# Kernel tuning notes

Hardware: AMD Instinct MI355X
Metric: run time of the kernel (lower is better)

Reference implementation:

```python
import jax, jax.numpy as jnp
import numpy as np

B, S, D, H, DFF = 8, 1024, 1024, 16, 4096
DK = D // H
NEG = -1000000000.0


def layernorm(x, g, b, eps=1e-5):
    mu = jnp.mean(x, axis=-1, keepdims=True)
    var = jnp.mean((x - mu) ** 2, axis=-1, keepdims=True)
    return (x - mu) / jnp.sqrt(var + eps) * g + b


def setup_inputs() -> dict:
    key = jax.random.key(0)
    ks = jax.random.split(key, 16)
    s = 0.02
    inp = {
        "x": jax.random.normal(ks[0], (B, S, D), jnp.float32),
        "binary_mask": jax.random.randint(ks[1], (B, S), 0, 2, jnp.int32),
        # per-head projections stacked: [H, D, DK]
        "Wq": jax.random.normal(ks[2], (H, D, DK), jnp.float32) * s,
        "bq": jnp.zeros((H, DK), jnp.float32),
        "Wk": jax.random.normal(ks[3], (H, D, DK), jnp.float32) * s,
        "bk": jnp.zeros((H, DK), jnp.float32),
        "Wv": jax.random.normal(ks[4], (H, D, DK), jnp.float32) * s,
        "bv": jnp.zeros((H, DK), jnp.float32),
        "Wo": jax.random.normal(ks[5], (D, D), jnp.float32) * s,
        "bo": jnp.zeros((D,), jnp.float32),
        "ga": jnp.ones((D,), jnp.float32),
        "ba": jnp.zeros((D,), jnp.float32),
        "W1": jax.random.normal(ks[6], (D, DFF), jnp.float32) * s,
        "b1": jnp.zeros((DFF,), jnp.float32),
        "W2": jax.random.normal(ks[7], (DFF, D), jnp.float32) * s,
        "b2": jnp.zeros((D,), jnp.float32),
        "gf": jnp.ones((D,), jnp.float32),
        "bf": jnp.zeros((D,), jnp.float32),
    }
    return inp


def encoder_fwd(x, binary_mask, Wq, bq, Wk, bk, Wv, bv, Wo, bo, ga, ba, W1, b1, W2, b2, gf, bf):
    # --- multi-head self-attention (heads vectorized over h axis) ---
    q = jnp.einsum("bsd,hdk->bhsk", x, Wq) + bq[None, :, None, :]
    k = jnp.einsum("bsd,hdk->bhsk", x, Wk) + bk[None, :, None, :]
    v = jnp.einsum("bsd,hdk->bhsk", x, Wv) + bv[None, :, None, :]
    score = jnp.einsum("bhik,bhjk->bhij", q, k) / jnp.sqrt(jnp.float32(DK))
    # mask: binary_mask is over KEY positions, broadcast over query dim
    score = score + jnp.where(binary_mask[:, None, None, :] == 0, NEG, 0.0)
    # NOTE: original code softmaxes over dim=1 of [B,Sq,Sk] -> the QUERY axis
    probs = jax.nn.softmax(score, axis=2)
    ctx = jnp.einsum("bhij,bhjk->bhik", probs, v)  # [B,H,S,DK]
    ctx = jnp.transpose(ctx, (0, 2, 1, 3)).reshape(x.shape[0], x.shape[1], D)
    attn_out = ctx @ Wo + bo
    y = layernorm(x + attn_out, ga, ba)
    # --- FFN ---
    h = jax.nn.relu(y @ W1 + b1)
    ffn_out = h @ W2 + b2
    return layernorm(y + ffn_out, gf, bf)


def reference(x, binary_mask, Wq, bq, Wk, bk, Wv, bv, Wo, bo, ga, ba, W1, b1, W2, b2, gf, bf):
    return encoder_fwd(x, binary_mask, Wq, bq, Wk, bk, Wv, bv, Wo, bo, ga, ba, W1, b1, W2, b2, gf, bf)
```

## Files before the change

### kernel.cpp

```cpp
#include <hip/hip_runtime.h>
#include <hip/hip_bf16.h>

typedef __bf16 bf16;
typedef __bf16 bf16x8 __attribute__((ext_vector_type(8)));
typedef __bf16 bf16x4 __attribute__((ext_vector_type(4)));
typedef float  f32x4  __attribute__((ext_vector_type(4)));

#define NB 8
#define NS 1024
#define ND 1024
#define NH 16
#define NDK 64
#define NDFF 4096

static __device__ __forceinline__ f32x4 mfma16(bf16x8 a, bf16x8 b, f32x4 c) {
    return __builtin_amdgcn_mfma_f32_16x16x32_bf16(a, b, c, 0, 0, 0);
}

#define GLDS(g, l) __builtin_amdgcn_global_load_lds( \
    (const __attribute__((address_space(1))) void*)(g), \
    (__attribute__((address_space(3))) void*)(l), 16, 0, 0)

__global__ __launch_bounds__(256) void cvt_x(const float* __restrict__ in,
                                             bf16* __restrict__ out, int n4)
{
    int idx = blockIdx.x * 256 + threadIdx.x;
    if (idx >= n4) return;
    float4 v = ((const float4*)in)[idx];
    bf16x4 o = { (bf16)v.x, (bf16)v.y, (bf16)v.z, (bf16)v.w };
    ((bf16x4*)out)[idx] = o;
}

__global__ __launch_bounds__(256) void prep_transpose(
    const float* __restrict__ Wq, const float* __restrict__ Wk, const float* __restrict__ Wv,
    const float* __restrict__ Wo, const float* __restrict__ W1, const float* __restrict__ W2,
    bf16* __restrict__ wqkvT, bf16* __restrict__ WoT,
    bf16* __restrict__ W1T, bf16* __restrict__ W2T)
{
    __shared__ float T[64][65];
    int bid = blockIdx.x;
    const float* src; bf16* dst; int srcLd, dstLd, tR, tC; bool scale = false;
    if (bid < 768) {
        int mat = bid >> 4, ty = bid & 15;
        int h = mat & 15, type = mat >> 4;
        const float* W = (type == 0) ? Wq : (type == 1 ? Wk : Wv);
        src = W + (size_t)h * ND * NDK;
        srcLd = NDK; tR = ty * 64; tC = 0;
        dst = wqkvT + ((size_t)type * 1024 + h * 64) * ND;
        dstLd = ND;
        scale = (type == 0);
    } else if (bid < 1024) {
        int b2 = bid - 768; int ty = b2 >> 4, tx = b2 & 15;
        src = Wo; srcLd = ND; tR = ty * 64; tC = tx * 64; dst = WoT; dstLd = ND;
    } else if (bid < 2048) {
        int b2 = bid - 1024; int ty = b2 >> 6, tx = b2 & 63;
        src = W1; srcLd = NDFF; tR = ty * 64; tC = tx * 64; dst = W1T; dstLd = ND;
    } else {
        int b2 = bid - 2048; int ty = b2 >> 4, tx = b2 & 15;
        src = W2; srcLd = ND; tR = ty * 64; tC = tx * 64; dst = W2T; dstLd = NDFF;
    }
    int t = threadIdx.x;
    int c0 = t & 63, r0 = t >> 6;
    #pragma unroll
    for (int rr = 0; rr < 16; rr++) {
        int row = rr * 4 + r0;
        T[row][c0] = src[(size_t)(tR + row) * srcLd + tC + c0];
    }
    __syncthreads();
    #pragma unroll
    for (int cc = 0; cc < 16; cc++) {
        int col = cc * 4 + r0;
        float v = T[c0][col];
        if (scale) v *= 0.125f;
        dst[(size_t)(tC + col) * dstLd + tR + c0] = (bf16)v;
    }
}

__global__ void prep_bias(const float* __restrict__ bq, const float* __restrict__ bk,
                          const float* __restrict__ bv, float* __restrict__ bqkv)
{
    int n = blockIdx.x * 256 + threadIdx.x;
    if (n >= 3072) return;
    int type = n >> 10, hk = n & 1023;
    const float* bb = (type == 0) ? bq : (type == 1 ? bk : bv);
    float v = bb[hk];
    if (type == 0) v *= 0.125f;
    bqkv[n] = v;
}

__device__ __forceinline__ void gemm_bt_core(
    const bf16* __restrict__ A, const bf16* __restrict__ BT, int K,
    int rowBase, int colBase, f32x4 (&acc)[4][4], bf16* As, bf16* Bs)
{
    const int tid = threadIdx.x;
    const int lane = tid & 63, wid = tid >> 6;
    const int wr = (wid >> 1) * 64, wc = (wid & 1) * 64;
    const int lrow = lane & 15, lq = lane >> 4;
    const int srow = wid * 32 + (lane >> 3);
    const int gblk = (lane & 7) ^ ((lane >> 3) & 7);
    const bf16* Arow = A + (size_t)(rowBase + srow) * K + gblk * 8;
    const bf16* Brow = BT + (size_t)(colBase + srow) * K + gblk * 8;
    const int co0 = ((lq) ^ (lrow & 7)) * 8;
    const int co1 = ((4 + lq) ^ (lrow & 7)) * 8;
    f32x4 zz = {0.f, 0.f, 0.f, 0.f};
    #pragma unroll
    for (int i = 0; i < 4; i++)
        #pragma unroll
        for (int j = 0; j < 4; j++) acc[i][j] = zz;
    for (int k0 = 0; k0 < K; k0 += 64) {
        __syncthreads();
        #pragma unroll
        for (int it = 0; it < 4; it++)
            GLDS(Arow + (size_t)it * 8 * K + k0, As + (wid * 32 + it * 8) * 64);
        #pragma unroll
        for (int it = 0; it < 4; it++)
            GLDS(Brow + (size_t)it * 8 * K + k0, Bs + (wid * 32 + it * 8) * 64);
        __syncthreads();
        #pragma unroll
        for (int kh = 0; kh < 2; kh++) {
            const int co = kh ? co1 : co0;
            bf16x8 af[4], bfr[4];
            #pragma unroll
            for (int tt = 0; tt < 4; tt++) {
                af[tt]  = *(const bf16x8*)&As[(wr + tt * 16 + lrow) * 64 + co];
                bfr[tt] = *(const bf16x8*)&Bs[(wc + tt * 16 + lrow) * 64 + co];
            }
            #pragma unroll
            for (int i = 0; i < 4; i++)
                #pragma unroll
                for (int j = 0; j < 4; j++)
                    acc[i][j] = mfma16(af[i], bfr[j], acc[i][j]);
        }
    }
}

__global__ __launch_bounds__(256) void g1_qkv(
    const bf16* __restrict__ x, const bf16* __restrict__ wqkvT, const float* __restrict__ bqkv,
    bf16* __restrict__ Q, bf16* __restrict__ Kb, bf16* __restrict__ Vb)
{
    __shared__ bf16 As[128 * 64], Bs[128 * 64];
    f32x4 acc[4][4];
    int rowBase = blockIdx.x * 128, colBase = blockIdx.y * 128;
    gemm_bt_core(x, wqkvT, ND, rowBase, colBase, acc, As, Bs);
    const int tid = threadIdx.x, lane = tid & 63, wid = tid >> 6;
    const int wr = (wid >> 1) * 64, wc = (wid & 1) * 64, lrow = lane & 15, lq = lane >> 4;
    #pragma unroll
    for (int j = 0; j < 4; j++) {
        int gcol = colBase + wc + j * 16 + lrow;
        float bias = bqkv[gcol];
        int type = gcol >> 10, h = (gcol >> 6) & 15, kk = gcol & 63;
        bf16* dst = (type == 0) ? Q : (type == 1 ? Kb : Vb);
        #pragma unroll
        for (int i = 0; i < 4; i++) {
            #pragma unroll
            for (int r = 0; r < 4; r++) {
                int grow = rowBase + wr + i * 16 + lq * 4 + r;
                int b = grow >> 10, s = grow & 1023;
                int bh = b * NH + h;
                dst[((size_t)bh * NS + s) * NDK + kk] = (bf16)(acc[i][j][r] + bias);
            }
        }
    }
}

__global__ __launch_bounds__(256) void vt_trans(
    const bf16* __restrict__ Vb, bf16* __restrict__ Vt)
{
    __shared__ bf16 T[64 * 72];
    int bh = blockIdx.y, s0 = blockIdx.x * 64;
    const bf16* src = Vb + ((size_t)bh * NS + s0) * NDK;
    int tid = threadIdx.x;
    #pragma unroll
    for (int it = 0; it < 2; it++) {
        int g = tid + it * 256;
        int row = g >> 3, c = (g & 7) * 8;
        *(bf16x8*)&T[row * 72 + c] = *(const bf16x8*)&src[row * NDK + c];
    }
    __syncthreads();
    #pragma unroll
    for (int it = 0; it < 2; it++) {
        int g = tid + it * 256;
        int kk = g >> 3, sc = (g & 7) * 8;
        bf16x8 v;
        #pragma unroll
        for (int t = 0; t < 8; t++) v[t] = T[(sc + t) * 72 + kk];
        *(bf16x8*)&Vt[((size_t)bh * NDK + kk) * NS + s0 + sc] = v;
    }
}

__global__ __launch_bounds__(256) void g2_stats(
    const bf16* __restrict__ Q, const bf16* __restrict__ Kb,
    const int* __restrict__ mask, float2* __restrict__ alpha)
{
    __shared__ bf16 Qs[64 * 64];
    int bh = blockIdx.y, b = bh >> 4;
    int jBase = blockIdx.x * 128;
    const bf16* Kp = Kb + (size_t)bh * NS * NDK;
    const bf16* Qp = Q + (size_t)bh * NS * NDK;
    const int tid = threadIdx.x, lane = tid & 63, wid = tid >> 6;
    const int lrow = lane & 15, lq = lane >> 4;
    bf16x8 kf[2][2];
    #pragma unroll
    for (int jt = 0; jt < 2; jt++)
        #pragma unroll
        for (int kh = 0; kh < 2; kh++)
            kf[jt][kh] = *(const bf16x8*)&Kp[(size_t)(jBase + wid * 32 + jt * 16 + lrow) * NDK + kh * 32 + lq * 8];
    const int srow = lane >> 3;
    const int gblk = (lane & 7) ^ srow;
    float Lacc[2][4];
    #pragma unroll
    for (int jt = 0; jt < 2; jt++)
        #pragma unroll
        for (int r = 0; r < 4; r++) Lacc[jt][r] = 0.f;
    f32x4 zz = {0.f, 0.f, 0.f, 0.f};
    for (int i0 = 0; i0 < NS; i0 += 64) {
        __syncthreads();
        #pragma unroll
        for (int it = 0; it < 2; it++)
            GLDS(Qp + (size_t)(i0 + wid * 16 + it * 8 + srow) * NDK + gblk * 8,
                 Qs + (wid * 16 + it * 8) * 64);
        __syncthreads();
        #pragma unroll
        for (int it = 0; it < 4; it++) {
            bf16x8 qb[2];
            #pragma unroll
            for (int kh = 0; kh < 2; kh++)
                qb[kh] = *(const bf16x8*)&Qs[(it * 16 + lrow) * 64 + ((kh * 4 + lq) ^ (lrow & 7)) * 8];
            #pragma unroll
            for (int jt = 0; jt < 2; jt++) {
                f32x4 s = mfma16(kf[jt][0], qb[0], zz);
                s = mfma16(kf[jt][1], qb[1], s);
                #pragma unroll
                for (int r = 0; r < 4; r++) Lacc[jt][r] += __expf(s[r]);
            }
        }
    }
    #pragma unroll
    for (int jt = 0; jt < 2; jt++) {
        #pragma unroll
        for (int r = 0; r < 4; r++) {
            float v = Lacc[jt][r];
            v += __shfl_xor(v, 1); v += __shfl_xor(v, 2);
            v += __shfl_xor(v, 4); v += __shfl_xor(v, 8);
            if (lrow == 0) {
                int j = jBase + wid * 32 + jt * 16 + lq * 4 + r;
                int m = mask[b * NS + j];
                float2 ac;
                ac.x = m ? 1.f / v : 0.f;
                ac.y = m ? 0.f : (1.f / 1024.f);
                alpha[(size_t)bh * NS + j] = ac;
            }
        }
    }
}

__global__ __launch_bounds__(256) void g3_ctx(
    const bf16* __restrict__ Q, const bf16* __restrict__ Kb, const bf16* __restrict__ Vt,
    const float2* __restrict__ alpha, bf16* __restrict__ ctx)
{
    __shared__ bf16 Ks[64 * 64];
    __shared__ bf16 Vs[64 * 64];
    __shared__ bf16 Ps[128 * 64];
    int bh = blockIdx.y, iBase = blockIdx.x * 128;
    int b = bh >> 4, h = bh & 15;
    const bf16* Qp = Q + (size_t)bh * NS * NDK;
    const bf16* Kp = Kb + (size_t)bh * NS * NDK;
    const bf16* Vp = Vt + (size_t)bh * NDK * NS;
    const float2* al = alpha + (size_t)bh * NS;
    const int tid = threadIdx.x, lane = tid & 63, wid = tid >> 6;
    const int lrow = lane & 15, lq = lane >> 4;
    const int wi = wid >> 1, wsub = wid & 1;
    bf16x8 qf[4][2];
    #pragma unroll
    for (int it = 0; it < 4; it++)
        #pragma unroll
        for (int kh = 0; kh < 2; kh++)
            qf[it][kh] = *(const bf16x8*)&Qp[(size_t)(iBase + wi * 64 + it * 16 + lrow) * NDK + kh * 32 + lq * 8];
    const int srow = lane >> 3;
    const int gblk = (lane & 7) ^ srow;
    f32x4 cacc[4][2];
    f32x4 zz = {0.f, 0.f, 0.f, 0.f};
    #pragma unroll
    for (int it = 0; it < 4; it++)
        #pragma unroll
        for (int kt = 0; kt < 2; kt++) cacc[it][kt] = zz;
    for (int j0 = 0; j0 < NS; j0 += 64) {
        __syncthreads();
        #pragma unroll
        for (int it = 0; it < 2; it++)
            GLDS(Kp + (size_t)(j0 + wid * 16 + it * 8 + srow) * NDK + gblk * 8,
                 Ks + (wid * 16 + it * 8) * 64);
        #pragma unroll
        for (int it = 0; it < 2; it++)
            GLDS(Vp + (size_t)(wid * 16 + it * 8 + srow) * NS + j0 + gblk * 8,
                 Vs + (wid * 16 + it * 8) * 64);
        __syncthreads();
        bf16x8 kb[2][2];
        #pragma unroll
        for (int jt = 0; jt < 2; jt++)
            #pragma unroll
            for (int kh = 0; kh < 2; kh++)
                kb[jt][kh] = *(const bf16x8*)&Ks[(wsub * 32 + jt * 16 + lrow) * 64 + ((kh * 4 + lq) ^ (lrow & 7)) * 8];
        float2 ac[2];
        ac[0] = al[j0 + wsub * 32 + lrow];
        ac[1] = al[j0 + wsub * 32 + 16 + lrow];
        #pragma unroll
        for (int it = 0; it < 4; it++) {
            #pragma unroll
            for (int jt = 0; jt < 2; jt++) {
                f32x4 s = mfma16(qf[it][0], kb[jt][0], zz);
                s = mfma16(qf[it][1], kb[jt][1], s);
                #pragma unroll
                for (int r = 0; r < 4; r++) {
                    float p = ac[jt].x * __expf(s[r]) + ac[jt].y;
                    int i = wi * 64 + it * 16 + lq * 4 + r;
                    int j = wsub * 32 + jt * 16 + lrow;
                    Ps[i * 64 + (((j >> 3) ^ (i & 7)) * 8) + (j & 7)] = (bf16)p;
                }
            }
        }
        __syncthreads();
        bf16x8 vb[2][2];
        #pragma unroll
        for (int kt = 0; kt < 2; kt++)
            #pragma unroll
            for (int kh = 0; kh < 2; kh++)
                vb[kt][kh] = *(const bf16x8*)&Vs[(wsub * 32 + kt * 16 + lrow) * 64 + ((kh * 4 + lq) ^ (lrow & 7)) * 8];
        #pragma unroll
        for (int it = 0; it < 4; it++) {
            bf16x8 pa[2];
            #pragma unroll
            for (int kh = 0; kh < 2; kh++)
                pa[kh] = *(const bf16x8*)&Ps[(wi * 64 + it * 16 + lrow) * 64 + ((kh * 4 + lq) ^ (lrow & 7)) * 8];
            #pragma unroll
            for (int kt = 0; kt < 2; kt++) {
                cacc[it][kt] = mfma16(pa[0], vb[kt][0], cacc[it][kt]);
                cacc[it][kt] = mfma16(pa[1], vb[kt][1], cacc[it][kt]);
            }
        }
    }
    #pragma unroll
    for (int kt = 0; kt < 2; kt++) {
        int col = h * NDK + wsub * 32 + kt * 16 + lrow;
        #pragma unroll
        for (int it = 0; it < 4; it++) {
            #pragma unroll
            for (int r = 0; r < 4; r++) {
                int i = iBase + wi * 64 + it * 16 + lq * 4 + r;
                ctx[(size_t)(b * NS + i) * ND + col] = (bf16)cacc[it][kt][r];
            }
        }
    }
}

__global__ __launch_bounds__(256) void g4_proj(
    const bf16* __restrict__ ctx, const bf16* __restrict__ WoT, const float* __restrict__ bo,
    const float* __restrict__ x, float* __restrict__ t1f)
{
    __shared__ bf16 As[128 * 64], Bs[128 * 64];
    f32x4 acc[4][4];
    int rowBase = blockIdx.x * 128, colBase = blockIdx.y * 128;
    gemm_bt_core(ctx, WoT, ND, rowBase, colBase, acc, As, Bs);
    const int tid = threadIdx.x, lane = tid & 63, wid = tid >> 6;
    const int wr = (wid >> 1) * 64, wc = (wid & 1) * 64, lrow = lane & 15, lq = lane >> 4;
    #pragma unroll
    for (int j = 0; j < 4; j++) {
        int gcol = colBase + wc + j * 16 + lrow;
        float bias = bo[gcol];
        #pragma unroll
        for (int i = 0; i < 4; i++) {
            #pragma unroll
            for (int r = 0; r < 4; r++) {
                int grow = rowBase + wr + i * 16 + lq * 4 + r;
                float v = acc[i][j][r] + bias + x[(size_t)grow * ND + gcol];
                t1f[(size_t)grow * ND + gcol] = v;
            }
        }
    }
}

__global__ __launch_bounds__(256) void g5_ffn1(
    const bf16* __restrict__ y, const bf16* __restrict__ W1T, const float* __restrict__ b1,
    bf16* __restrict__ hb)
{
    __shared__ bf16 As[128 * 64], Bs[128 * 64];
    f32x4 acc[4][4];
    int rowBase = blockIdx.x * 128, colBase = blockIdx.y * 128;
    gemm_bt_core(y, W1T, ND, rowBase, colBase, acc, As, Bs);
    const int tid = threadIdx.x, lane = tid & 63, wid = tid >> 6;
    const int wr = (wid >> 1) * 64, wc = (wid & 1) * 64, lrow = lane & 15, lq = lane >> 4;
    #pragma unroll
    for (int j = 0; j < 4; j++) {
        int gcol = colBase + wc + j * 16 + lrow;
        float bias = b1[gcol];
        #pragma unroll
        for (int i = 0; i < 4; i++) {
            #pragma unroll
            for (int r = 0; r < 4; r++) {
                int grow = rowBase + wr + i * 16 + lq * 4 + r;
                float v = fmaxf(acc[i][j][r] + bias, 0.f);
                hb[(size_t)grow * NDFF + gcol] = (bf16)v;
            }
        }
    }
}

__global__ __launch_bounds__(256) void g6_ffn2(
    const bf16* __restrict__ hb, const bf16* __restrict__ W2T, const float* __restrict__ b2,
    const float* __restrict__ yf, float* __restrict__ zf)
{
    __shared__ bf16 As[128 * 64], Bs[128 * 64];
    f32x4 acc[4][4];
    int rowBase = blockIdx.x * 128, colBase = blockIdx.y * 128;
    gemm_bt_core(hb, W2T, NDFF, rowBase, colBase, acc, As, Bs);
    const int tid = threadIdx.x, lane = tid & 63, wid = tid >> 6;
    const int wr = (wid >> 1) * 64, wc = (wid & 1) * 64, lrow = lane & 15, lq = lane >> 4;
    #pragma unroll
    for (int j = 0; j < 4; j++) {
        int gcol = colBase + wc + j * 16 + lrow;
        float bias = b2[gcol];
        #pragma unroll
        for (int i = 0; i < 4; i++) {
            #pragma unroll
            for (int r = 0; r < 4; r++) {
                int grow = rowBase + wr + i * 16 + lq * 4 + r;
                float v = acc[i][j][r] + bias + yf[(size_t)grow * ND + gcol];
                zf[(size_t)grow * ND + gcol] = v;
            }
        }
    }
}

__global__ __launch_bounds__(256) void ln_kernel(
    const float* __restrict__ in, float* __restrict__ outf, bf16* __restrict__ outb,
    const float* __restrict__ g, const float* __restrict__ bb)
{
    int row = blockIdx.x, tid = threadIdx.x;
    const float* p = in + (size_t)row * ND;
    float4 v4 = ((const float4*)p)[tid];
    float s = v4.x + v4.y + v4.z + v4.w;
    float q = v4.x * v4.x + v4.y * v4.y + v4.z * v4.z + v4.w * v4.w;
    #pragma unroll
    for (int m = 1; m < 64; m <<= 1) { s += __shfl_xor(s, m); q += __shfl_xor(q, m); }
    __shared__ float rs[4], rq[4];
    int wid = tid >> 6, lane = tid & 63;
    if (lane == 0) { rs[wid] = s; rq[wid] = q; }
    __syncthreads();
    s = rs[0] + rs[1] + rs[2] + rs[3];
    q = rq[0] + rq[1] + rq[2] + rq[3];
    float mean = s * (1.f / 1024.f);
    float var = q * (1.f / 1024.f) - mean * mean;
    float rstd = 1.f / sqrtf(var + 1e-5f);
    float vv[4] = {v4.x, v4.y, v4.z, v4.w};
    float4 of;
    bf16x4 ob;
    #pragma unroll
    for (int k = 0; k < 4; k++) {
        int col = tid * 4 + k;
        float yv = (vv[k] - mean) * rstd * g[col] + bb[col];
        ((float*)&of)[k] = yv;
        ob[k] = (bf16)yv;
    }
    ((float4*)(outf + (size_t)row * ND))[tid] = of;
    if (outb) *(bf16x4*)&outb[(size_t)row * ND + tid * 4] = ob;
}

extern "C" void kernel_launch(void* const* d_in, const int* in_sizes, int n_in,
                              void* d_out, int out_size, void* d_ws, size_t ws_size,
                              hipStream_t stream)
{
    const float* x    = (const float*)d_in[0];
    const int*   mask = (const int*)d_in[1];
    const float* Wq   = (const float*)d_in[2];
    const float* bq   = (const float*)d_in[3];
    const float* Wk   = (const float*)d_in[4];
    const float* bk   = (const float*)d_in[5];
    const float* Wv   = (const float*)d_in[6];
    const float* bv   = (const float*)d_in[7];
    const float* Wo   = (const float*)d_in[8];
    const float* bo   = (const float*)d_in[9];
    const float* ga   = (const float*)d_in[10];
    const float* ba   = (const float*)d_in[11];
    const float* W1   = (const float*)d_in[12];
    const float* b1   = (const float*)d_in[13];
    const float* W2   = (const float*)d_in[14];
    const float* b2   = (const float*)d_in[15];
    const float* gf   = (const float*)d_in[16];
    const float* bfb  = (const float*)d_in[17];

    size_t off = 0;
    auto alloc = [&](size_t n) { char* p = (char*)d_ws + off; off += (n + 255) & ~(size_t)255; return (void*)p; };
    bf16*   wqkvT = (bf16*)  alloc((size_t)3072 * 1024 * 2);
    bf16*   WoT   = (bf16*)  alloc((size_t)1024 * 1024 * 2);
    bf16*   W1T   = (bf16*)  alloc((size_t)4096 * 1024 * 2);
    bf16*   W2T   = (bf16*)  alloc((size_t)1024 * 4096 * 2);
    float*  bqkv  = (float*) alloc(3072 * 4);
    float2* alpha = (float2*)alloc((size_t)NB * NH * NS * 8);
    bf16*   xb    = (bf16*)  alloc((size_t)8192 * 1024 * 2);
    bf16*   ub    = (bf16*)  alloc((size_t)8192 * 4096 * 2);
    bf16*   Qb    = ub;
    bf16*   Kb    = ub + (size_t)8192 * 1024;
    bf16*   Vt    = ub + (size_t)2 * 8192 * 1024;
    bf16*   ctx   = ub + (size_t)3 * 8192 * 1024;
    bf16*   hb    = ub;
    float*  t1f   = (float*) alloc((size_t)8192 * 1024 * 4);
    float*  zf    = t1f;
    bf16*   Vb    = (bf16*)t1f;
    bf16*   yb    = (bf16*)  alloc((size_t)8192 * 1024 * 2);
    float*  yf    = (float*) alloc((size_t)8192 * 1024 * 4);

    cvt_x<<<8192, 256, 0, stream>>>(x, xb, 8192 * 1024 / 4);
    prep_transpose<<<3072, 256, 0, stream>>>(Wq, Wk, Wv, Wo, W1, W2, wqkvT, WoT, W1T, W2T);
    prep_bias<<<12, 256, 0, stream>>>(bq, bk, bv, bqkv);
    g1_qkv<<<dim3(64, 24), 256, 0, stream>>>(xb, wqkvT, bqkv, Qb, Kb, Vb);
    vt_trans<<<dim3(16, 128), 256, 0, stream>>>(Vb, Vt);
    g2_stats<<<dim3(8, 128), 256, 0, stream>>>(Qb, Kb, mask, alpha);
    g3_ctx<<<dim3(8, 128), 256, 0, stream>>>(Qb, Kb, Vt, alpha, ctx);
    g4_proj<<<dim3(64, 8), 256, 0, stream>>>(ctx, WoT, bo, x, t1f);
    ln_kernel<<<8192, 256, 0, stream>>>(t1f, yf, yb, ga, ba);
    g5_ffn1<<<dim3(64, 32), 256, 0, stream>>>(yb, W1T, b1, hb);
    g6_ffn2<<<dim3(64, 8), 256, 0, stream>>>(hb, W2T, b2, yf, zf);
    ln_kernel<<<8192, 256, 0, stream>>>(zf, (float*)d_out, nullptr, gf, bfb);
}
```

Measured before the change: 529.0 us.

## Store residual and LayerNorm intermediates in bf16 and widen attention tiles

The residual-plus-projection buffers (t1, z) and the first LayerNorm output are now kept only in bf16 instead of fp32, and the residual add reads the bf16 copy of x. This roughly halves memory traffic for the epilogues and LayerNorm passes and drops one fp32 buffer. The attention stats kernel now loads 128 query rows per LDS stage. The context kernel gives each wave its own 64-row query tile with a private P buffer over all 64 keys, which removes one block barrier per key step. The trade-off is extra bf16 rounding in the residual path and higher register and LDS use per block.

```diff
diff --git a/kernel.cpp b/kernel.cpp
--- a/kernel.cpp
+++ b/kernel.cpp
@@ -156,8 +156,7 @@
             for (int r = 0; r < 4; r++) {
                 int grow = rowBase + wr + i * 16 + lq * 4 + r;
                 int b = grow >> 10, s = grow & 1023;
-                int bh = b * NH + h;
-                dst[((size_t)bh * NS + s) * NDK + kk] = (bf16)(acc[i][j][r] + bias);
+                dst[((size_t)(b * NH + h) * NS + s) * NDK + kk] = (bf16)(acc[i][j][r] + bias);
             }
         }
     }
@@ -192,7 +191,7 @@
     const bf16* __restrict__ Q, const bf16* __restrict__ Kb,
     const int* __restrict__ mask, float2* __restrict__ alpha)
 {
-    __shared__ bf16 Qs[64 * 64];
+    __shared__ bf16 Qs[128 * 64];
     int bh = blockIdx.y, b = bh >> 4;
     int jBase = blockIdx.x * 128;
     const bf16* Kp = Kb + (size_t)bh * NS * NDK;
@@ -213,15 +212,15 @@
         #pragma unroll
         for (int r = 0; r < 4; r++) Lacc[jt][r] = 0.f;
     f32x4 zz = {0.f, 0.f, 0.f, 0.f};
-    for (int i0 = 0; i0 < NS; i0 += 64) {
+    for (int i0 = 0; i0 < NS; i0 += 128) {
         __syncthreads();
         #pragma unroll
-        for (int it = 0; it < 2; it++)
-            GLDS(Qp + (size_t)(i0 + wid * 16 + it * 8 + srow) * NDK + gblk * 8,
-                 Qs + (wid * 16 + it * 8) * 64);
+        for (int it = 0; it < 4; it++)
+            GLDS(Qp + (size_t)(i0 + wid * 32 + it * 8 + srow) * NDK + gblk * 8,
+                 Qs + (wid * 32 + it * 8) * 64);
         __syncthreads();
         #pragma unroll
-        for (int it = 0; it < 4; it++) {
+        for (int it = 0; it < 8; it++) {
             bf16x8 qb[2];
             #pragma unroll
             for (int kh = 0; kh < 2; kh++)
@@ -260,8 +259,8 @@
 {
     __shared__ bf16 Ks[64 * 64];
     __shared__ bf16 Vs[64 * 64];
-    __shared__ bf16 Ps[128 * 64];
-    int bh = blockIdx.y, iBase = blockIdx.x * 128;
+    __shared__ bf16 Ps[4 * 64 * 64];
+    int bh = blockIdx.y, iBase = blockIdx.x * 256;
     int b = bh >> 4, h = bh & 15;
     const bf16* Qp = Q + (size_t)bh * NS * NDK;
     const bf16* Kp = Kb + (size_t)bh * NS * NDK;
@@ -269,21 +268,22 @@
     const float2* al = alpha + (size_t)bh * NS;
     const int tid = threadIdx.x, lane = tid & 63, wid = tid >> 6;
     const int lrow = lane & 15, lq = lane >> 4;
-    const int wi = wid >> 1, wsub = wid & 1;
+    const int iw = iBase + wid * 64;
     bf16x8 qf[4][2];
     #pragma unroll
     for (int it = 0; it < 4; it++)
         #pragma unroll
         for (int kh = 0; kh < 2; kh++)
-            qf[it][kh] = *(const bf16x8*)&Qp[(size_t)(iBase + wi * 64 + it * 16 + lrow) * NDK + kh * 32 + lq * 8];
+            qf[it][kh] = *(const bf16x8*)&Qp[(size_t)(iw + it * 16 + lrow) * NDK + kh * 32 + lq * 8];
     const int srow = lane >> 3;
     const int gblk = (lane & 7) ^ srow;
-    f32x4 cacc[4][2];
+    f32x4 cacc[4][4];
     f32x4 zz = {0.f, 0.f, 0.f, 0.f};
     #pragma unroll
     for (int it = 0; it < 4; it++)
         #pragma unroll
-        for (int kt = 0; kt < 2; kt++) cacc[it][kt] = zz;
+        for (int kt = 0; kt < 4; kt++) cacc[it][kt] = zz;
+    bf16* Pw = Ps + wid * 64 * 64;
     for (int j0 = 0; j0 < NS; j0 += 64) {
         __syncthreads();
         #pragma unroll
@@ -295,58 +295,57 @@
             GLDS(Vp + (size_t)(wid * 16 + it * 8 + srow) * NS + j0 + gblk * 8,
                  Vs + (wid * 16 + it * 8) * 64);
         __syncthreads();
-        bf16x8 kb[2][2];
-        #pragma unroll
-        for (int jt = 0; jt < 2; jt++)
+        bf16x8 kb[4][2];
+        #pragma unroll
+        for (int jt = 0; jt < 4; jt++)
             #pragma unroll
             for (int kh = 0; kh < 2; kh++)
-                kb[jt][kh] = *(const bf16x8*)&Ks[(wsub * 32 + jt * 16 + lrow) * 64 + ((kh * 4 + lq) ^ (lrow & 7)) * 8];
-        float2 ac[2];
-        ac[0] = al[j0 + wsub * 32 + lrow];
-        ac[1] = al[j0 + wsub * 32 + 16 + lrow];
-        #pragma unroll
-        for (int it = 0; it < 4; it++) {
-            #pragma unroll
-            for (int jt = 0; jt < 2; jt++) {
-                f32x4 s = mfma16(qf[it][0], kb[jt][0], zz);
-                s = mfma16(qf[it][1], kb[jt][1], s);
+                kb[jt][kh] = *(const bf16x8*)&Ks[(jt * 16 + lrow) * 64 + ((kh * 4 + lq) ^ (lrow & 7)) * 8];
+        #pragma unroll
+        for (int jt = 0; jt < 4; jt++) {
+            float2 acj[4];
+            #pragma unroll
+            for (int r = 0; r < 4; r++) acj[r] = al[j0 + jt * 16 + lq * 4 + r];
+            #pragma unroll
+            for (int it = 0; it < 4; it++) {
+                f32x4 s = mfma16(kb[jt][0], qf[it][0], zz);
+                s = mfma16(kb[jt][1], qf[it][1], s);
+                bf16x4 pv;
                 #pragma unroll
-                for (int r = 0; r < 4; r++) {
-                    float p = ac[jt].x * __expf(s[r]) + ac[jt].y;
-                    int i = wi * 64 + it * 16 + lq * 4 + r;
-                    int j = wsub * 32 + jt * 16 + lrow;
-                    Ps[i * 64 + (((j >> 3) ^ (i & 7)) * 8) + (j & 7)] = (bf16)p;
-                }
-            }
-        }
-        __syncthreads();
-        bf16x8 vb[2][2];
-        #pragma unroll
-        for (int kt = 0; kt < 2; kt++)
+                for (int r = 0; r < 4; r++)
+                    pv[r] = (bf16)(acj[r].x * __expf(s[r]) + acj[r].y);
+                int i = it * 16 + lrow;
+                int jb = jt * 2 + (lq >> 1);
+                *(bf16x4*)&Pw[i * 64 + ((jb ^ (i & 7)) * 8) + (lq & 1) * 4] = pv;
+            }
+        }
+        bf16x8 vb[4][2];
+        #pragma unroll
+        for (int kt = 0; kt < 4; kt++)
             #pragma unroll
             for (int kh = 0; kh < 2; kh++)
-                vb[kt][kh] = *(const bf16x8*)&Vs[(wsub * 32 + kt * 16 + lrow) * 64 + ((kh * 4 + lq) ^ (lrow & 7)) * 8];
+                vb[kt][kh] = *(const bf16x8*)&Vs[(kt * 16 + lrow) * 64 + ((kh * 4 + lq) ^ (lrow & 7)) * 8];
         #pragma unroll
         for (int it = 0; it < 4; it++) {
             bf16x8 pa[2];
             #pragma unroll
             for (int kh = 0; kh < 2; kh++)
-                pa[kh] = *(const bf16x8*)&Ps[(wi * 64 + it * 16 + lrow) * 64 + ((kh * 4 + lq) ^ (lrow & 7)) * 8];
-            #pragma unroll
-            for (int kt = 0; kt < 2; kt++) {
+                pa[kh] = *(const bf16x8*)&Pw[(it * 16 + lrow) * 64 + ((kh * 4 + lq) ^ (lrow & 7)) * 8];
+            #pragma unroll
+            for (int kt = 0; kt < 4; kt++) {
                 cacc[it][kt] = mfma16(pa[0], vb[kt][0], cacc[it][kt]);
                 cacc[it][kt] = mfma16(pa[1], vb[kt][1], cacc[it][kt]);
             }
         }
     }
     #pragma unroll
-    for (int kt = 0; kt < 2; kt++) {
-        int col = h * NDK + wsub * 32 + kt * 16 + lrow;
+    for (int kt = 0; kt < 4; kt++) {
+        int col = h * NDK + kt * 16 + lrow;
         #pragma unroll
         for (int it = 0; it < 4; it++) {
             #pragma unroll
             for (int r = 0; r < 4; r++) {
-                int i = iBase + wi * 64 + it * 16 + lq * 4 + r;
+                int i = iw + it * 16 + lq * 4 + r;
                 ctx[(size_t)(b * NS + i) * ND + col] = (bf16)cacc[it][kt][r];
             }
         }
@@ -355,7 +354,7 @@
 
 __global__ __launch_bounds__(256) void g4_proj(
     const bf16* __restrict__ ctx, const bf16* __restrict__ WoT, const float* __restrict__ bo,
-    const float* __restrict__ x, float* __restrict__ t1f)
+    const bf16* __restrict__ xb, bf16* __restrict__ t1b)
 {
     __shared__ bf16 As[128 * 64], Bs[128 * 64];
     f32x4 acc[4][4];
@@ -372,8 +371,8 @@
             #pragma unroll
             for (int r = 0; r < 4; r++) {
                 int grow = rowBase + wr + i * 16 + lq * 4 + r;
-                float v = acc[i][j][r] + bias + x[(size_t)grow * ND + gcol];
-                t1f[(size_t)grow * ND + gcol] = v;
+                float v = acc[i][j][r] + bias + (float)xb[(size_t)grow * ND + gcol];
+                t1b[(size_t)grow * ND + gcol] = (bf16)v;
             }
         }
     }
@@ -407,7 +406,7 @@
 
 __global__ __launch_bounds__(256) void g6_ffn2(
     const bf16* __restrict__ hb, const bf16* __restrict__ W2T, const float* __restrict__ b2,
-    const float* __restrict__ yf, float* __restrict__ zf)
+    const bf16* __restrict__ yb, bf16* __restrict__ zb)
 {
     __shared__ bf16 As[128 * 64], Bs[128 * 64];
     f32x4 acc[4][4];
@@ -424,22 +423,23 @@
             #pragma unroll
             for (int r = 0; r < 4; r++) {
                 int grow = rowBase + wr + i * 16 + lq * 4 + r;
-                float v = acc[i][j][r] + bias + yf[(size_t)grow * ND + gcol];
-                zf[(size_t)grow * ND + gcol] = v;
+                float v = acc[i][j][r] + bias + (float)yb[(size_t)grow * ND + gcol];
+                zb[(size_t)grow * ND + gcol] = (bf16)v;
             }
         }
     }
 }
 
 __global__ __launch_bounds__(256) void ln_kernel(
-    const float* __restrict__ in, float* __restrict__ outf, bf16* __restrict__ outb,
+    const bf16* __restrict__ in, bf16* __restrict__ outb, float* __restrict__ outf,
     const float* __restrict__ g, const float* __restrict__ bb)
 {
     int row = blockIdx.x, tid = threadIdx.x;
-    const float* p = in + (size_t)row * ND;
-    float4 v4 = ((const float4*)p)[tid];
-    float s = v4.x + v4.y + v4.z + v4.w;
-    float q = v4.x * v4.x + v4.y * v4.y + v4.z * v4.z + v4.w * v4.w;
+    const bf16* p = in + (size_t)row * ND;
+    bf16x4 v4 = *(const bf16x4*)&p[tid * 4];
+    float vv[4] = {(float)v4[0], (float)v4[1], (float)v4[2], (float)v4[3]};
+    float s = vv[0] + vv[1] + vv[2] + vv[3];
+    float q = vv[0]*vv[0] + vv[1]*vv[1] + vv[2]*vv[2] + vv[3]*vv[3];
     #pragma unroll
     for (int m = 1; m < 64; m <<= 1) { s += __shfl_xor(s, m); q += __shfl_xor(q, m); }
     __shared__ float rs[4], rq[4];
@@ -451,7 +451,6 @@
     float mean = s * (1.f / 1024.f);
     float var = q * (1.f / 1024.f) - mean * mean;
     float rstd = 1.f / sqrtf(var + 1e-5f);
-    float vv[4] = {v4.x, v4.y, v4.z, v4.w};
     float4 of;
     bf16x4 ob;
     #pragma unroll
@@ -461,8 +460,8 @@
         ((float*)&of)[k] = yv;
         ob[k] = (bf16)yv;
     }
-    ((float4*)(outf + (size_t)row * ND))[tid] = of;
     if (outb) *(bf16x4*)&outb[(size_t)row * ND + tid * 4] = ob;
+    if (outf) ((float4*)(outf + (size_t)row * ND))[tid] = of;
 }
 
 extern "C" void kernel_launch(void* const* d_in, const int* in_sizes, int n_in,
@@ -503,11 +502,10 @@
     bf16*   Vt    = ub + (size_t)2 * 8192 * 1024;
     bf16*   ctx   = ub + (size_t)3 * 8192 * 1024;
     bf16*   hb    = ub;
-    float*  t1f   = (float*) alloc((size_t)8192 * 1024 * 4);
-    float*  zf    = t1f;
-    bf16*   Vb    = (bf16*)t1f;
+    bf16*   t1b   = (bf16*)  alloc((size_t)8192 * 1024 * 2);
+    bf16*   Vb    = t1b;
+    bf16*   zb    = t1b;
     bf16*   yb    = (bf16*)  alloc((size_t)8192 * 1024 * 2);
-    float*  yf    = (float*) alloc((size_t)8192 * 1024 * 4);
 
     cvt_x<<<8192, 256, 0, stream>>>(x, xb, 8192 * 1024 / 4);
     prep_transpose<<<3072, 256, 0, stream>>>(Wq, Wk, Wv, Wo, W1, W2, wqkvT, WoT, W1T, W2T);
@@ -515,10 +513,10 @@
     g1_qkv<<<dim3(64, 24), 256, 0, stream>>>(xb, wqkvT, bqkv, Qb, Kb, Vb);
     vt_trans<<<dim3(16, 128), 256, 0, stream>>>(Vb, Vt);
     g2_stats<<<dim3(8, 128), 256, 0, stream>>>(Qb, Kb, mask, alpha);
-    g3_ctx<<<dim3(8, 128), 256, 0, stream>>>(Qb, Kb, Vt, alpha, ctx);
-    g4_proj<<<dim3(64, 8), 256, 0, stream>>>(ctx, WoT, bo, x, t1f);
-    ln_kernel<<<8192, 256, 0, stream>>>(t1f, yf, yb, ga, ba);
+    g3_ctx<<<dim3(4, 128), 256, 0, stream>>>(Qb, Kb, Vt, alpha, ctx);
+    g4_proj<<<dim3(64, 8), 256, 0, stream>>>(ctx, WoT, bo, xb, t1b);
+    ln_kernel<<<8192, 256, 0, stream>>>(t1b, yb, nullptr, ga, ba);
     g5_ffn1<<<dim3(64, 32), 256, 0, stream>>>(yb, W1T, b1, hb);
-    g6_ffn2<<<dim3(64, 8), 256, 0, stream>>>(hb, W2T, b2, yf, zf);
-    ln_kernel<<<8192, 256, 0, stream>>>(zf, (float*)d_out, nullptr, gf, bfb);
-}
+    g6_ffn2<<<dim3(64, 8), 256, 0, stream>>>(hb, W2T, b2, yb, zb);
+    ln_kernel<<<8192, 256, 0, stream>>>(zb, nullptr, (float*)d_out, gf, bfb);
+}
```

Result: faster. 501.9 us (-5.1%).
